# Kernel optimization log

Hardware: AMD Instinct MI355X
Metric: run time of the kernel (lower is better)

Reference implementation:

```python
import jax, jax.numpy as jnp
import numpy as np

N, E = 50000, 400000
F_IN, F_E = 128, 32
H, C = 4, 64          # heads, out_channels per head (concat=False -> head mean)
NUM_CLASSES = 16
BN_EPS = 1e-5


def setup_inputs() -> dict:
    key = jax.random.key(0)
    ks = jax.random.split(key, 16)
    s = 0.05
    return {
        "x": jax.random.normal(ks[0], (N, F_IN), jnp.float32),
        "edge_index": jax.random.randint(ks[1], (2, E), 0, N, jnp.int64),
        "edge_attr": jax.random.normal(ks[2], (E, F_E), jnp.float32),
        # TransformerConv params
        "Wq": jax.random.normal(ks[3], (F_IN, H * C), jnp.float32) * s,
        "bq": jnp.zeros((H * C,), jnp.float32),
        "Wk": jax.random.normal(ks[4], (F_IN, H * C), jnp.float32) * s,
        "bk": jnp.zeros((H * C,), jnp.float32),
        "Wv": jax.random.normal(ks[5], (F_IN, H * C), jnp.float32) * s,
        "bv": jnp.zeros((H * C,), jnp.float32),
        "We": jax.random.normal(ks[6], (F_E, H * C), jnp.float32) * s,  # lin_edge, no bias
        "Wskip": jax.random.normal(ks[7], (F_IN, C), jnp.float32) * s,   # root weight (concat=False -> C)
        "bskip": jnp.zeros((C,), jnp.float32),
        # BatchNorm1d (eval mode: running stats)
        "gamma": jnp.ones((C,), jnp.float32),
        "beta": jnp.zeros((C,), jnp.float32),
        "run_mean": jnp.zeros((C,), jnp.float32),
        "run_var": jnp.ones((C,), jnp.float32),
        # classifier
        "Wc": jax.random.normal(ks[8], (C, NUM_CLASSES), jnp.float32) * s,
        "bc": jnp.zeros((NUM_CLASSES,), jnp.float32),
    }


def reference(x, edge_index, edge_attr, Wq, bq, Wk, bk, Wv, bv, We,
              Wskip, bskip, gamma, beta, run_mean, run_var, Wc, bc):
    src = edge_index[0]  # j (message source)
    dst = edge_index[1]  # i (message target / softmax segment)

    q = (x @ Wq + bq).reshape(N, H, C)
    k = (x @ Wk + bk).reshape(N, H, C)
    v = (x @ Wv + bv).reshape(N, H, C)
    e = (edge_attr @ We).reshape(E, H, C)

    k_j = k[src] + e                                   # [E,H,C]
    score = jnp.sum(q[dst] * k_j, axis=-1) / jnp.sqrt(jnp.float32(C))  # [E,H]

    # segment softmax over incoming edges of each destination node
    m = jax.ops.segment_max(score, dst, num_segments=N)      # [N,H]
    ex = jnp.exp(score - m[dst])                             # [E,H]
    denom = jax.ops.segment_sum(ex, dst, num_segments=N)[dst]
    alpha = ex / denom                                       # [E,H]

    msg = (v[src] + e) * alpha[..., None]                    # [E,H,C]
    out = jax.ops.segment_sum(msg, dst, num_segments=N)      # [N,H,C]
    out = out.mean(axis=1)                                   # concat=False -> head mean [N,C]
    out = out + x @ Wskip + bskip                            # root/skip connection

    out = jax.nn.relu(out)
    # dropout: eval mode -> identity
    out = (out - run_mean) / jnp.sqrt(run_var + BN_EPS) * gamma + beta
    return out @ Wc + bc
```

## Files before the change

kernel.cpp:

```cpp
#include <hip/hip_runtime.h>
#include <hip/hip_bf16.h>

#define H 4
#define C 64
#define HC 256
#define FIN 128
#define FE 32
#define NCLS 16
#define BN_EPS 1e-5f
#define WCOLS 960

typedef __hip_bfloat16 bf16;
typedef __attribute__((ext_vector_type(8))) short short8v;
typedef __attribute__((ext_vector_type(4))) short short4v;
typedef __attribute__((ext_vector_type(2))) short short2v;
typedef __attribute__((ext_vector_type(4))) float floatx4;

__device__ __forceinline__ float b2f(bf16 v) { return __bfloat162float(v); }
__device__ __forceinline__ float bs2f(short s) {
    unsigned u = ((unsigned)(unsigned short)s) << 16;
    return __uint_as_float(u);
}
__device__ __forceinline__ short f2bs(float f) {
    bf16 h = __float2bfloat16(f);
    return *reinterpret_cast<short*>(&h);
}

__global__ __launch_bounds__(128) void pack_w_kernel(
    const float* __restrict__ Wq, const float* __restrict__ Wk, const float* __restrict__ Wv,
    const float* __restrict__ We, const float* __restrict__ Wskip,
    const float* __restrict__ bq, const float* __restrict__ bk, const float* __restrict__ bv,
    const float* __restrict__ bskip,
    const float* __restrict__ gamma, const float* __restrict__ beta,
    const float* __restrict__ rmean, const float* __restrict__ rvar,
    const float* __restrict__ Wc,
    short* __restrict__ Wt, float* __restrict__ bias,
    short* __restrict__ Wet, short* __restrict__ Wct,
    float* __restrict__ scalev, float* __restrict__ shiftv)
{
    const int bid = blockIdx.x;
    const int t = threadIdx.x;
    if (bid < WCOLS) {
        const int col = bid;
        float val, b = 0.f;
        if (col < 256)      { val = Wq[t * HC + col]; b = bq[col]; }
        else if (col < 512) { val = Wk[t * HC + col - 256]; b = bk[col - 256]; }
        else if (col < 768) { val = Wv[t * HC + col - 512]; b = bv[col - 512]; }
        else if (col < 896) {
            int j = col - 768, h = j >> 5, f = j & 31;
            float acc = 0.f;
#pragma unroll 8
            for (int c = 0; c < C; ++c) acc += Wq[t * HC + h * C + c] * We[f * HC + h * C + c];
            val = acc;
            acc = 0.f;
            for (int c = 0; c < C; ++c) acc += bq[h * C + c] * We[f * HC + h * C + c];
            b = acc;
        }
        else { int c2 = col - 896; val = Wskip[t * C + c2]; b = bskip[c2]; }
        Wt[(size_t)col * FIN + t] = f2bs(val);
        if (t == 0) bias[col] = b;
    } else if (bid < WCOLS + 64) {
        const int c2 = bid - WCOLS;
        const int f = t & 31, h = t >> 5;
        Wet[(size_t)c2 * FIN + t] = f2bs(We[f * HC + h * C + c2]);
    } else if (bid < WCOLS + 64 + NCLS) {
        const int cls = bid - WCOLS - 64;
        if (t < C) Wct[(size_t)cls * C + t] = f2bs(Wc[t * NCLS + cls]);
    } else {
        if (t < C) {
            float inv = rsqrtf(rvar[t] + BN_EPS);
            float sc = gamma[t] * inv;
            scalev[t] = sc;
            shiftv[t] = beta[t] - rmean[t] * sc;
        }
    }
}

__global__ __launch_bounds__(256) void qkv_mfma_kernel(
    const float* __restrict__ x, const short* __restrict__ Wt,
    const float* __restrict__ bias,
    bf16* __restrict__ q, unsigned char* __restrict__ kv,
    bf16* __restrict__ qWe, bf16* __restrict__ skip, int N)
{
    const int wid = threadIdx.x >> 6;
    const int lane = threadIdx.x & 63;
    const int n0 = blockIdx.x * 32;
    const int arow = lane & 15, agrp = lane >> 4;
    __shared__ __align__(16) unsigned char kvs[32][512];

    short8v afrag[2][4];
#pragma unroll
    for (int rt = 0; rt < 2; ++rt) {
        int nA = n0 + rt * 16 + arow; if (nA >= N) nA = N - 1;
        const float* xrow = x + (size_t)nA * FIN + agrp * 8;
#pragma unroll
        for (int ks = 0; ks < 4; ++ks) {
            floatx4 x0 = *(const floatx4*)(xrow + ks * 32);
            floatx4 x1 = *(const floatx4*)(xrow + ks * 32 + 4);
            short8v a;
            a[0] = f2bs(x0[0]); a[1] = f2bs(x0[1]); a[2] = f2bs(x0[2]); a[3] = f2bs(x0[3]);
            a[4] = f2bs(x1[0]); a[5] = f2bs(x1[1]); a[6] = f2bs(x1[2]); a[7] = f2bs(x1[3]);
            afrag[rt][ks] = a;
        }
    }

    for (int ct = wid; ct < WCOLS / 16; ct += 4) {
        const int col0 = ct * 16;
        const int col = col0 + arow;
        const short* wp = Wt + (size_t)col * FIN + agrp * 8;
        short8v bfr[4];
#pragma unroll
        for (int ks = 0; ks < 4; ++ks) bfr[ks] = *(const short8v*)(wp + ks * 32);
        floatx4 acc0 = {0.f, 0.f, 0.f, 0.f};
        floatx4 acc1 = {0.f, 0.f, 0.f, 0.f};
#pragma unroll
        for (int ks = 0; ks < 4; ++ks) {
            acc0 = __builtin_amdgcn_mfma_f32_16x16x32_bf16(afrag[0][ks], bfr[ks], acc0, 0, 0, 0);
            acc1 = __builtin_amdgcn_mfma_f32_16x16x32_bf16(afrag[1][ks], bfr[ks], acc1, 0, 0, 0);
        }
        const float bb = bias[col];
#pragma unroll
        for (int rt = 0; rt < 2; ++rt) {
            const floatx4 acc = rt ? acc1 : acc0;
#pragma unroll
            for (int r = 0; r < 4; ++r) {
                const int row = rt * 16 + agrp * 4 + r;
                const int n = n0 + row;
                const float val = acc[r] + bb;
                if (col0 >= 256 && col0 < 768) {
                    int c = col - 256;
                    const int isv = (c >= 256) ? 4 : 0;
                    c &= 255;
                    const int pos = ((c >> 6) * 16 + ((c & 63) >> 2)) * 8 + (c & 3) + isv;
                    const int p8 = __builtin_amdgcn_cvt_pk_fp8_f32(val, val, 0, false);
                    kvs[row][pos] = (unsigned char)(p8 & 0xff);
                } else if (n < N) {
                    if (col0 < 256)      q[(size_t)n * HC + col]          = __float2bfloat16(val);
                    else if (col0 < 896) qWe[(size_t)n * 128 + col - 768] = __float2bfloat16(val);
                    else                 skip[(size_t)n * C + col - 896]  = __float2bfloat16(val);
                }
            }
        }
    }
    __syncthreads();
    const int t = threadIdx.x;
#pragma unroll
    for (int it = 0; it < 4; ++it) {
        const int lin = it * 256 + t;
        const int row = lin >> 5;
        const int ch  = lin & 31;
        const int n = n0 + row;
        if (n < N)
            *(uint4*)(kv + (size_t)n * 512 + ch * 16) = *(const uint4*)(&kvs[row][ch * 16]);
    }
}

__global__ __launch_bounds__(256) void hist_kernel(
    const int* __restrict__ dst, int* __restrict__ deg, int E)
{
    const int i = blockIdx.x * 256 + threadIdx.x;
    if (i < E) atomicAdd(&deg[dst[i]], 1);
}

__global__ __launch_bounds__(256) void partial_kernel(
    const int* __restrict__ deg, int* __restrict__ partials, int N)
{
    const int t = threadIdx.x;
    const int base = blockIdx.x * 1024 + t * 4;
    int s = 0;
#pragma unroll
    for (int i = 0; i < 4; ++i) {
        int idx = base + i;
        if (idx < N) s += deg[idx];
    }
#pragma unroll
    for (int off = 1; off < 64; off <<= 1) s += __shfl_xor(s, off, 64);
    __shared__ int ws[4];
    if ((t & 63) == 0) ws[t >> 6] = s;
    __syncthreads();
    if (t == 0) partials[blockIdx.x] = ws[0] + ws[1] + ws[2] + ws[3];
}

__global__ __launch_bounds__(256) void scan_partials_kernel(
    int* __restrict__ partials, int* __restrict__ rowptr, int nb, int N)
{
    const int t = threadIdx.x;
    __shared__ int sm[256];
    int v = (t < nb) ? partials[t] : 0;
    sm[t] = v;
    __syncthreads();
    for (int off = 1; off < 256; off <<= 1) {
        int vv = (t >= off) ? sm[t - off] : 0;
        __syncthreads();
        sm[t] += vv;
        __syncthreads();
    }
    if (t < nb) partials[t] = sm[t] - v;
    if (t == 255) rowptr[N] = sm[255];
}

__global__ __launch_bounds__(256) void write_rowptr_kernel(
    const int* __restrict__ deg, const int* __restrict__ partials,
    int* __restrict__ rowptr, int N)
{
    const int t = threadIdx.x;
    const int base = blockIdx.x * 1024 + t * 4;
    int d[4];
    int s = 0;
#pragma unroll
    for (int i = 0; i < 4; ++i) {
        int idx = base + i;
        d[i] = (idx < N) ? deg[idx] : 0;
        s += d[i];
    }
    __shared__ int sm[256];
    sm[t] = s;
    __syncthreads();
    for (int off = 1; off < 256; off <<= 1) {
        int vv = (t >= off) ? sm[t - off] : 0;
        __syncthreads();
        sm[t] += vv;
        __syncthreads();
    }
    int run = partials[blockIdx.x] + sm[t] - s;
#pragma unroll
    for (int i = 0; i < 4; ++i) {
        int idx = base + i;
        if (idx < N) { rowptr[idx] = run; run += d[i]; }
    }
}

__global__ __launch_bounds__(256) void scatter_kernel(
    const int* __restrict__ src, const int* __restrict__ dst,
    const int* __restrict__ rowptr, int* __restrict__ cnt2,
    int2* __restrict__ edg, int E)
{
    const int i = blockIdx.x * 256 + threadIdx.x;
    if (i >= E) return;
    const int d = dst[i];
    const int pos = rowptr[d] + atomicAdd(&cnt2[d], 1);
    edg[pos] = make_int2(src[i], i);
}

__global__ __launch_bounds__(256) void node_agg_kernel(
    const int2* __restrict__ edg, const int* __restrict__ rowptr,
    const float* __restrict__ ea,
    const bf16* __restrict__ q, const unsigned char* __restrict__ kv,
    const bf16* __restrict__ qWe,
    float* __restrict__ accV, bf16* __restrict__ aggEA, int N)
{
    const int w = threadIdx.x >> 6;
    const int lane = threadIdx.x & 63;
    const int d = blockIdx.x * 4 + w;
    if (d >= N) return;
    const int g = lane >> 4;
    const int li = lane & 15;
    const int kvoff = (g * 16 + li) * 8;

    short4v qs = *(const short4v*)((const short*)q + (size_t)d * HC + g * C + li * 4);
    const float qv0 = bs2f(qs[0]), qv1 = bs2f(qs[1]), qv2 = bs2f(qs[2]), qv3 = bs2f(qs[3]);
    short2v qws = *(const short2v*)((const short*)qWe + (size_t)d * 128 + g * FE + li * 2);
    const float qw0 = bs2f(qws[0]), qw1 = bs2f(qws[1]);

    float den = 0.f;
    float a0 = 0.f, a1 = 0.f, a2 = 0.f, a3 = 0.f;
    float ag0 = 0.f, ag1 = 0.f;

    const int beg = rowptr[d];
    const int degc = rowptr[d + 1] - beg;

    for (int c0 = 0; c0 < degc; c0 += 64) {
        const int cnt = min(degc - c0, 64);
        int2 me = make_int2(0, 0);
        if (lane < cnt) me = edg[beg + c0 + lane];

        const int s0 = __builtin_amdgcn_readlane(me.x, 0);
        const int e0i = __builtin_amdgcn_readlane(me.y, 0);
        uint2 kvv = *(const uint2*)(kv + (size_t)s0 * 512 + kvoff);
        float2 eaf = *(const float2*)(ea + (size_t)e0i * FE + li * 2);

        for (int j = 0; j < cnt; ++j) {
            uint2 kvn = kvv; float2 ean = eaf;
            if (j + 1 < cnt) {
                const int sn = __builtin_amdgcn_readlane(me.x, j + 1);
                const int en = __builtin_amdgcn_readlane(me.y, j + 1);
                kvn = *(const uint2*)(kv + (size_t)sn * 512 + kvoff);
                ean = *(const float2*)(ea + (size_t)en * FE + li * 2);
            }
            const float ea0 = eaf.x, ea1 = eaf.y;
            const int klo = (int)kvv.x, vhi = (int)kvv.y;
            float p = qv0 * __builtin_amdgcn_cvt_f32_fp8(klo, 0)
                    + qv1 * __builtin_amdgcn_cvt_f32_fp8(klo, 1)
                    + qv2 * __builtin_amdgcn_cvt_f32_fp8(klo, 2)
                    + qv3 * __builtin_amdgcn_cvt_f32_fp8(klo, 3)
                    + qw0 * ea0 + qw1 * ea1;
            p += __shfl_xor(p, 1, 64);
            p += __shfl_xor(p, 2, 64);
            p += __shfl_xor(p, 4, 64);
            p += __shfl_xor(p, 8, 64);
            const float e = exp2f(p * 0.18033688f);
            den += e;
            a0 += e * __builtin_amdgcn_cvt_f32_fp8(vhi, 0);
            a1 += e * __builtin_amdgcn_cvt_f32_fp8(vhi, 1);
            a2 += e * __builtin_amdgcn_cvt_f32_fp8(vhi, 2);
            a3 += e * __builtin_amdgcn_cvt_f32_fp8(vhi, 3);
            ag0 += e * ea0; ag1 += e * ea1;
            kvv = kvn; eaf = ean;
        }
    }

    const float inv = den > 0.f ? 0.25f / den : 0.f;
    a0 *= inv; a1 *= inv; a2 *= inv; a3 *= inv;
    a0 += __shfl_xor(a0, 16, 64); a0 += __shfl_xor(a0, 32, 64);
    a1 += __shfl_xor(a1, 16, 64); a1 += __shfl_xor(a1, 32, 64);
    a2 += __shfl_xor(a2, 16, 64); a2 += __shfl_xor(a2, 32, 64);
    a3 += __shfl_xor(a3, 16, 64); a3 += __shfl_xor(a3, 32, 64);
    if (g == 0) {
        floatx4 o = {a0, a1, a2, a3};
        *(floatx4*)(accV + (size_t)d * C + li * 4) = o;
    }
    short2v so;
    so[0] = f2bs(ag0 * inv);
    so[1] = f2bs(ag1 * inv);
    *(short2v*)((short*)aggEA + (size_t)d * 128 + g * FE + li * 2) = so;
}

__global__ __launch_bounds__(256) void final_kernel(
    const bf16* __restrict__ aggEA, const float* __restrict__ accV,
    const bf16* __restrict__ skip,
    const short* __restrict__ Wet, const short* __restrict__ Wct,
    const float* __restrict__ scalev, const float* __restrict__ shiftv,
    const float* __restrict__ bc,
    float* __restrict__ out, int N)
{
    const int wid = threadIdx.x >> 6;
    const int lane = threadIdx.x & 63;
    const int n0 = blockIdx.x * 16;
    const int arow = lane & 15, agrp = lane >> 4;
    __shared__ short hs[16][72];

    int nA = n0 + arow; if (nA >= N) nA = N - 1;
    const short* ap = (const short*)aggEA + (size_t)nA * 128 + agrp * 8;
    const int c0 = wid * 16;
    const int col = c0 + arow;
    const short* wp = Wet + (size_t)col * FIN + agrp * 8;
    floatx4 acc = {0.f, 0.f, 0.f, 0.f};
#pragma unroll
    for (int ks = 0; ks < 4; ++ks) {
        short8v a = *(const short8v*)(ap + ks * 32);
        short8v b = *(const short8v*)(wp + ks * 32);
        acc = __builtin_amdgcn_mfma_f32_16x16x32_bf16(a, b, acc, 0, 0, 0);
    }
    const float sc = scalev[col], sh = shiftv[col];
#pragma unroll
    for (int r = 0; r < 4; ++r) {
        const int row = agrp * 4 + r;
        int n = n0 + row; int nc = (n < N) ? n : (N - 1);
        float z = acc[r] + accV[(size_t)nc * C + col] + b2f(skip[(size_t)nc * C + col]);
        z = fmaxf(z, 0.f);
        z = z * sc + sh;
        hs[row][col] = f2bs(z);
    }
    __syncthreads();

    if (wid == 0) {
        short8v ah[2], bh[2];
#pragma unroll
        for (int ks = 0; ks < 2; ++ks) {
#pragma unroll
            for (int j = 0; j < 8; ++j) ah[ks][j] = hs[arow][ks * 32 + agrp * 8 + j];
            bh[ks] = *(const short8v*)(Wct + (size_t)arow * C + ks * 32 + agrp * 8);
        }
        floatx4 co = {0.f, 0.f, 0.f, 0.f};
        co = __builtin_amdgcn_mfma_f32_16x16x32_bf16(ah[0], bh[0], co, 0, 0, 0);
        co = __builtin_amdgcn_mfma_f32_16x16x32_bf16(ah[1], bh[1], co, 0, 0, 0);
        const float bcv = bc[arow];
#pragma unroll
        for (int r = 0; r < 4; ++r) {
            const int n = n0 + agrp * 4 + r;
            if (n < N) out[(size_t)n * NCLS + arow] = co[r] + bcv;
        }
    }
}

extern "C" void kernel_launch(void* const* d_in, const int* in_sizes, int n_in,
                              void* d_out, int out_size, void* d_ws, size_t ws_size,
                              hipStream_t stream)
{
    const float* x     = (const float*)d_in[0];
    const int*   ei    = (const int*)d_in[1];
    const float* ea    = (const float*)d_in[2];
    const float* Wq    = (const float*)d_in[3];
    const float* bq    = (const float*)d_in[4];
    const float* Wk    = (const float*)d_in[5];
    const float* bk    = (const float*)d_in[6];
    const float* Wv    = (const float*)d_in[7];
    const float* bv    = (const float*)d_in[8];
    const float* We    = (const float*)d_in[9];
    const float* Wskip = (const float*)d_in[10];
    const float* bskip = (const float*)d_in[11];
    const float* gamma = (const float*)d_in[12];
    const float* beta  = (const float*)d_in[13];
    const float* rmean = (const float*)d_in[14];
    const float* rvar  = (const float*)d_in[15];
    const float* Wc    = (const float*)d_in[16];
    const float* bc    = (const float*)d_in[17];
    float* out = (float*)d_out;

    const int N = in_sizes[0] / FIN;
    const int E = in_sizes[2] / FE;
    const int* srcp = ei;
    const int* dstp = ei + E;
    const int nb = (N + 1023) / 1024;

    char* w = (char*)d_ws;
    size_t off = 0;
    auto alloc = [&](size_t bytes) { void* p = w + off; off += (bytes + 255) & ~255ull; return p; };
    bf16*  qb     = (bf16*)alloc((size_t)N * HC * sizeof(bf16));
    unsigned char* kvbuf = (unsigned char*)alloc((size_t)N * 512);
    bf16*  qWe    = (bf16*)alloc((size_t)N * 128 * sizeof(bf16));
    bf16*  skip   = (bf16*)alloc((size_t)N * C * sizeof(bf16));
    int*   deg    = (int*)alloc((size_t)N * sizeof(int));
    int*   rowptr = (int*)alloc((size_t)(N + 1) * sizeof(int));
    int*   cnt2   = (int*)alloc((size_t)N * sizeof(int));
    int*   partials = (int*)alloc(256 * sizeof(int));
    int2*  edg    = (int2*)alloc((size_t)E * sizeof(int2));
    float* accV   = (float*)alloc((size_t)N * C * sizeof(float));
    bf16*  aggEA  = (bf16*)alloc((size_t)N * 128 * sizeof(bf16));
    short* Wt     = (short*)alloc((size_t)WCOLS * FIN * sizeof(short));
    float* bias   = (float*)alloc((size_t)WCOLS * sizeof(float));
    short* Wet    = (short*)alloc((size_t)C * FIN * sizeof(short));
    short* Wct    = (short*)alloc((size_t)NCLS * C * sizeof(short));
    float* scalev = (float*)alloc((size_t)C * sizeof(float));
    float* shiftv = (float*)alloc((size_t)C * sizeof(float));

    hipMemsetAsync(deg,  0, (size_t)N * sizeof(int), stream);
    hipMemsetAsync(cnt2, 0, (size_t)N * sizeof(int), stream);

    pack_w_kernel<<<WCOLS + 64 + NCLS + 1, 128, 0, stream>>>(
        Wq, Wk, Wv, We, Wskip, bq, bk, bv, bskip, gamma, beta, rmean, rvar, Wc,
        Wt, bias, Wet, Wct, scalev, shiftv);
    qkv_mfma_kernel<<<(N + 31) / 32, 256, 0, stream>>>(x, Wt, bias, qb, kvbuf, qWe, skip, N);
    hist_kernel<<<(E + 255) / 256, 256, 0, stream>>>(dstp, deg, E);
    partial_kernel<<<nb, 256, 0, stream>>>(deg, partials, N);
    scan_partials_kernel<<<1, 256, 0, stream>>>(partials, rowptr, nb, N);
    write_rowptr_kernel<<<nb, 256, 0, stream>>>(deg, partials, rowptr, N);
    scatter_kernel<<<(E + 255) / 256, 256, 0, stream>>>(srcp, dstp, rowptr, cnt2, edg, E);
    node_agg_kernel<<<(N + 3) / 4, 256, 0, stream>>>(edg, rowptr, ea, qb, kvbuf, qWe, accV, aggEA, N);
    final_kernel<<<(N + 15) / 16, 256, 0, stream>>>(aggEA, accV, skip, Wet, Wct, scalev, shiftv, bc, out, N);
}
```

Before: 199.0 us.

## Split interleaved fp8 K/V buffer into separate planes and prefetch weight fragments

Replaces the interleaved fp8 KV layout staged through shared memory with two separate row-major fp8 planes for K and V, written directly from the MFMA accumulators. This removes the LDS staging buffer and the block barrier in the projection kernel. The projection loop now loads the next column tile's weight fragments before the current MFMAs run. In exchange, the aggregation kernel issues two 4-byte gathers per edge instead of one 8-byte gather, and the projection kernel's K/V stores become scattered byte stores.

```diff
diff --git a/kernel.cpp b/kernel.cpp
--- a/kernel.cpp
+++ b/kernel.cpp
@@ -79,14 +79,13 @@
 __global__ __launch_bounds__(256) void qkv_mfma_kernel(
     const float* __restrict__ x, const short* __restrict__ Wt,
     const float* __restrict__ bias,
-    bf16* __restrict__ q, unsigned char* __restrict__ kv,
+    bf16* __restrict__ q, unsigned char* __restrict__ kpl, unsigned char* __restrict__ vpl,
     bf16* __restrict__ qWe, bf16* __restrict__ skip, int N)
 {
     const int wid = threadIdx.x >> 6;
     const int lane = threadIdx.x & 63;
     const int n0 = blockIdx.x * 32;
     const int arow = lane & 15, agrp = lane >> 4;
-    __shared__ __align__(16) unsigned char kvs[32][512];
 
     short8v afrag[2][4];
 #pragma unroll
@@ -104,13 +103,28 @@
         }
     }
 
-    for (int ct = wid; ct < WCOLS / 16; ct += 4) {
+    int ct = wid;
+    short8v bfr[4];
+    {
+        const short* wp = Wt + (size_t)(ct * 16 + arow) * FIN + agrp * 8;
+#pragma unroll
+        for (int ks = 0; ks < 4; ++ks) bfr[ks] = *(const short8v*)(wp + ks * 32);
+    }
+
+    while (ct < WCOLS / 16) {
+        const int ctn = ct + 4;
+        short8v bfn[4];
+        if (ctn < WCOLS / 16) {
+            const short* wp = Wt + (size_t)(ctn * 16 + arow) * FIN + agrp * 8;
+#pragma unroll
+            for (int ks = 0; ks < 4; ++ks) bfn[ks] = *(const short8v*)(wp + ks * 32);
+        } else {
+#pragma unroll
+            for (int ks = 0; ks < 4; ++ks) bfn[ks] = bfr[ks];
+        }
+
         const int col0 = ct * 16;
         const int col = col0 + arow;
-        const short* wp = Wt + (size_t)col * FIN + agrp * 8;
-        short8v bfr[4];
-#pragma unroll
-        for (int ks = 0; ks < 4; ++ks) bfr[ks] = *(const short8v*)(wp + ks * 32);
         floatx4 acc0 = {0.f, 0.f, 0.f, 0.f};
         floatx4 acc1 = {0.f, 0.f, 0.f, 0.f};
 #pragma unroll
@@ -119,39 +133,71 @@
             acc1 = __builtin_amdgcn_mfma_f32_16x16x32_bf16(afrag[1][ks], bfr[ks], acc1, 0, 0, 0);
         }
         const float bb = bias[col];
-#pragma unroll
-        for (int rt = 0; rt < 2; ++rt) {
-            const floatx4 acc = rt ? acc1 : acc0;
-#pragma unroll
-            for (int r = 0; r < 4; ++r) {
-                const int row = rt * 16 + agrp * 4 + r;
-                const int n = n0 + row;
-                const float val = acc[r] + bb;
-                if (col0 >= 256 && col0 < 768) {
-                    int c = col - 256;
-                    const int isv = (c >= 256) ? 4 : 0;
-                    c &= 255;
-                    const int pos = ((c >> 6) * 16 + ((c & 63) >> 2)) * 8 + (c & 3) + isv;
-                    const int p8 = __builtin_amdgcn_cvt_pk_fp8_f32(val, val, 0, false);
-                    kvs[row][pos] = (unsigned char)(p8 & 0xff);
-                } else if (n < N) {
-                    if (col0 < 256)      q[(size_t)n * HC + col]          = __float2bfloat16(val);
-                    else if (col0 < 896) qWe[(size_t)n * 128 + col - 768] = __float2bfloat16(val);
-                    else                 skip[(size_t)n * C + col - 896]  = __float2bfloat16(val);
+
+        if (col0 < 256) {
+#pragma unroll
+            for (int rt = 0; rt < 2; ++rt) {
+                const floatx4 acc = rt ? acc1 : acc0;
+#pragma unroll
+                for (int r = 0; r < 4; ++r) {
+                    const int n = n0 + rt * 16 + agrp * 4 + r;
+                    if (n < N) q[(size_t)n * HC + col] = __float2bfloat16(acc[r] + bb);
                 }
             }
-        }
-    }
-    __syncthreads();
-    const int t = threadIdx.x;
-#pragma unroll
-    for (int it = 0; it < 4; ++it) {
-        const int lin = it * 256 + t;
-        const int row = lin >> 5;
-        const int ch  = lin & 31;
-        const int n = n0 + row;
-        if (n < N)
-            *(uint4*)(kv + (size_t)n * 512 + ch * 16) = *(const uint4*)(&kvs[row][ch * 16]);
+        } else if (col0 < 512) {
+            const int c = col - 256;
+#pragma unroll
+            for (int rt = 0; rt < 2; ++rt) {
+                const floatx4 acc = rt ? acc1 : acc0;
+#pragma unroll
+                for (int r = 0; r < 4; ++r) {
+                    const int n = n0 + rt * 16 + agrp * 4 + r;
+                    if (n < N) {
+                        const int p8 = __builtin_amdgcn_cvt_pk_fp8_f32(acc[r] + bb, acc[r] + bb, 0, false);
+                        kpl[(size_t)n * 256 + c] = (unsigned char)(p8 & 0xff);
+                    }
+                }
+            }
+        } else if (col0 < 768) {
+            const int c = col - 512;
+#pragma unroll
+            for (int rt = 0; rt < 2; ++rt) {
+                const floatx4 acc = rt ? acc1 : acc0;
+#pragma unroll
+                for (int r = 0; r < 4; ++r) {
+                    const int n = n0 + rt * 16 + agrp * 4 + r;
+                    if (n < N) {
+                        const int p8 = __builtin_amdgcn_cvt_pk_fp8_f32(acc[r] + bb, acc[r] + bb, 0, false);
+                        vpl[(size_t)n * 256 + c] = (unsigned char)(p8 & 0xff);
+                    }
+                }
+            }
+        } else if (col0 < 896) {
+            const int c = col - 768;
+#pragma unroll
+            for (int rt = 0; rt < 2; ++rt) {
+                const floatx4 acc = rt ? acc1 : acc0;
+#pragma unroll
+                for (int r = 0; r < 4; ++r) {
+                    const int n = n0 + rt * 16 + agrp * 4 + r;
+                    if (n < N) qWe[(size_t)n * 128 + c] = __float2bfloat16(acc[r] + bb);
+                }
+            }
+        } else {
+            const int c = col - 896;
+#pragma unroll
+            for (int rt = 0; rt < 2; ++rt) {
+                const floatx4 acc = rt ? acc1 : acc0;
+#pragma unroll
+                for (int r = 0; r < 4; ++r) {
+                    const int n = n0 + rt * 16 + agrp * 4 + r;
+                    if (n < N) skip[(size_t)n * C + c] = __float2bfloat16(acc[r] + bb);
+                }
+            }
+        }
+#pragma unroll
+        for (int ks = 0; ks < 4; ++ks) bfr[ks] = bfn[ks];
+        ct = ctn;
     }
 }
 
@@ -245,7 +291,8 @@
 __global__ __launch_bounds__(256) void node_agg_kernel(
     const int2* __restrict__ edg, const int* __restrict__ rowptr,
     const float* __restrict__ ea,
-    const bf16* __restrict__ q, const unsigned char* __restrict__ kv,
+    const bf16* __restrict__ q,
+    const unsigned char* __restrict__ kpl, const unsigned char* __restrict__ vpl,
     const bf16* __restrict__ qWe,
     float* __restrict__ accV, bf16* __restrict__ aggEA, int N)
 {
@@ -255,7 +302,7 @@
     if (d >= N) return;
     const int g = lane >> 4;
     const int li = lane & 15;
-    const int kvoff = (g * 16 + li) * 8;
+    const int koff = g * 64 + li * 4;
 
     short4v qs = *(const short4v*)((const short*)q + (size_t)d * HC + g * C + li * 4);
     const float qv0 = bs2f(qs[0]), qv1 = bs2f(qs[1]), qv2 = bs2f(qs[2]), qv3 = bs2f(qs[3]);
@@ -276,23 +323,24 @@
 
         const int s0 = __builtin_amdgcn_readlane(me.x, 0);
         const int e0i = __builtin_amdgcn_readlane(me.y, 0);
-        uint2 kvv = *(const uint2*)(kv + (size_t)s0 * 512 + kvoff);
+        unsigned kw = *(const unsigned*)(kpl + (size_t)s0 * 256 + koff);
+        unsigned vw = *(const unsigned*)(vpl + (size_t)s0 * 256 + koff);
         float2 eaf = *(const float2*)(ea + (size_t)e0i * FE + li * 2);
 
         for (int j = 0; j < cnt; ++j) {
-            uint2 kvn = kvv; float2 ean = eaf;
+            unsigned kwn = kw, vwn = vw; float2 ean = eaf;
             if (j + 1 < cnt) {
                 const int sn = __builtin_amdgcn_readlane(me.x, j + 1);
                 const int en = __builtin_amdgcn_readlane(me.y, j + 1);
-                kvn = *(const uint2*)(kv + (size_t)sn * 512 + kvoff);
+                kwn = *(const unsigned*)(kpl + (size_t)sn * 256 + koff);
+                vwn = *(const unsigned*)(vpl + (size_t)sn * 256 + koff);
                 ean = *(const float2*)(ea + (size_t)en * FE + li * 2);
             }
             const float ea0 = eaf.x, ea1 = eaf.y;
-            const int klo = (int)kvv.x, vhi = (int)kvv.y;
-            float p = qv0 * __builtin_amdgcn_cvt_f32_fp8(klo, 0)
-                    + qv1 * __builtin_amdgcn_cvt_f32_fp8(klo, 1)
-                    + qv2 * __builtin_amdgcn_cvt_f32_fp8(klo, 2)
-                    + qv3 * __builtin_amdgcn_cvt_f32_fp8(klo, 3)
+            float p = qv0 * __builtin_amdgcn_cvt_f32_fp8((int)kw, 0)
+                    + qv1 * __builtin_amdgcn_cvt_f32_fp8((int)kw, 1)
+                    + qv2 * __builtin_amdgcn_cvt_f32_fp8((int)kw, 2)
+                    + qv3 * __builtin_amdgcn_cvt_f32_fp8((int)kw, 3)
                     + qw0 * ea0 + qw1 * ea1;
             p += __shfl_xor(p, 1, 64);
             p += __shfl_xor(p, 2, 64);
@@ -300,12 +348,12 @@
             p += __shfl_xor(p, 8, 64);
             const float e = exp2f(p * 0.18033688f);
             den += e;
-            a0 += e * __builtin_amdgcn_cvt_f32_fp8(vhi, 0);
-            a1 += e * __builtin_amdgcn_cvt_f32_fp8(vhi, 1);
-            a2 += e * __builtin_amdgcn_cvt_f32_fp8(vhi, 2);
-            a3 += e * __builtin_amdgcn_cvt_f32_fp8(vhi, 3);
+            a0 += e * __builtin_amdgcn_cvt_f32_fp8((int)vw, 0);
+            a1 += e * __builtin_amdgcn_cvt_f32_fp8((int)vw, 1);
+            a2 += e * __builtin_amdgcn_cvt_f32_fp8((int)vw, 2);
+            a3 += e * __builtin_amdgcn_cvt_f32_fp8((int)vw, 3);
             ag0 += e * ea0; ag1 += e * ea1;
-            kvv = kvn; eaf = ean;
+            kw = kwn; vw = vwn; eaf = ean;
         }
     }
 
@@ -417,7 +465,8 @@
     size_t off = 0;
     auto alloc = [&](size_t bytes) { void* p = w + off; off += (bytes + 255) & ~255ull; return p; };
     bf16*  qb     = (bf16*)alloc((size_t)N * HC * sizeof(bf16));
-    unsigned char* kvbuf = (unsigned char*)alloc((size_t)N * 512);
+    unsigned char* kpl = (unsigned char*)alloc((size_t)N * 256);
+    unsigned char* vpl = (unsigned char*)alloc((size_t)N * 256);
     bf16*  qWe    = (bf16*)alloc((size_t)N * 128 * sizeof(bf16));
     bf16*  skip   = (bf16*)alloc((size_t)N * C * sizeof(bf16));
     int*   deg    = (int*)alloc((size_t)N * sizeof(int));
@@ -440,12 +489,12 @@
     pack_w_kernel<<<WCOLS + 64 + NCLS + 1, 128, 0, stream>>>(
         Wq, Wk, Wv, We, Wskip, bq, bk, bv, bskip, gamma, beta, rmean, rvar, Wc,
         Wt, bias, Wet, Wct, scalev, shiftv);
-    qkv_mfma_kernel<<<(N + 31) / 32, 256, 0, stream>>>(x, Wt, bias, qb, kvbuf, qWe, skip, N);
+    qkv_mfma_kernel<<<(N + 31) / 32, 256, 0, stream>>>(x, Wt, bias, qb, kpl, vpl, qWe, skip, N);
     hist_kernel<<<(E + 255) / 256, 256, 0, stream>>>(dstp, deg, E);
     partial_kernel<<<nb, 256, 0, stream>>>(deg, partials, N);
     scan_partials_kernel<<<1, 256, 0, stream>>>(partials, rowptr, nb, N);
     write_rowptr_kernel<<<nb, 256, 0, stream>>>(deg, partials, rowptr, N);
     scatter_kernel<<<(E + 255) / 256, 256, 0, stream>>>(srcp, dstp, rowptr, cnt2, edg, E);
-    node_agg_kernel<<<(N + 3) / 4, 256, 0, stream>>>(edg, rowptr, ea, qb, kvbuf, qWe, accV, aggEA, N);
+    node_agg_kernel<<<(N + 3) / 4, 256, 0, stream>>>(edg, rowptr, ea, qb, kpl, vpl, qWe, accV, aggEA, N);
     final_kernel<<<(N + 15) / 16, 256, 0, stream>>>(aggEA, accV, skip, Wet, Wct, scalev, shiftv, bc, out, N);
 }
```

Result: slower. 220.7 us (+10.9%).
